# Optimization experiments

Measured on AMD Instinct MI355X. Metric: run time of the kernel, lower is better.

Reference implementation:

```python
import jax, jax.numpy as jnp
import numpy as np

TOP_K = 2


def setup_inputs() -> dict:
    key = jax.random.key(0)
    ks = jax.random.split(key, 5)
    B, S, D, F, E = 2, 2048, 1024, 3584, 8
    scale_in = 1.0 / np.sqrt(D)
    scale_ff = 1.0 / np.sqrt(F)
    return {
        "hidden_states": jax.random.normal(ks[0], (B, S, D), dtype=jnp.float32),
        "gate_w": jax.random.normal(ks[1], (E, D), dtype=jnp.float32) * scale_in,
        "w1": jax.random.normal(ks[2], (E, F, D), dtype=jnp.float32) * scale_in,
        "w3": jax.random.normal(ks[3], (E, F, D), dtype=jnp.float32) * scale_in,
        "w2": jax.random.normal(ks[4], (E, D, F), dtype=jnp.float32) * scale_ff,
    }


def reference(hidden_states, gate_w, w1, w3, w2):
    B, S, D = hidden_states.shape
    E = gate_w.shape[0]
    x = hidden_states.reshape(-1, D)                      # [T, D]
    T = x.shape[0]
    router_logits = x @ gate_w.T                          # [T, E]
    probs = jax.nn.softmax(router_logits.astype(jnp.float32), axis=-1)
    top_w, sel = jax.lax.top_k(probs, TOP_K)              # [T, K]
    top_w = top_w / jnp.sum(top_w, axis=-1, keepdims=True)
    top_w = top_w.astype(x.dtype)
    # per-token per-expert combine weight (scatter top-k weights to dense [T, E])
    w_full = jnp.zeros((T, E), dtype=x.dtype).at[jnp.arange(T)[:, None], sel].add(top_w)
    # Original scales the INPUT by the routing weight before the SwiGLU expert;
    # tokens not routed to expert e have weight 0 -> MLP_e(0) == 0 (no biases),
    # so a dense per-expert pass summed over experts reproduces the gather/scatter exactly.
    out = jnp.zeros_like(x)
    for e in range(E):  # fixed small expert count
        xs = x * w_full[:, e:e + 1]                       # [T, D]
        h = jax.nn.silu(xs @ w1[e].T) * (xs @ w3[e].T)    # [T, F]
        out = out + h @ w2[e].T                           # [T, D]
    return out.reshape(B, S, D), router_logits
```

## Files before the change

### kernel.cpp

```cpp
#include <hip/hip_runtime.h>


#define T_TOK 4096
#define D_DIM 1024
#define F_DIM 3584
#define E_NUM 8
#define N13   (2 * F_DIM)
#define BM 128
#define BN 128
#define BK 32
#define LDK (BK + 8)
#define MAXROWS (2 * T_TOK + E_NUM * (BM - 1) + 8)

typedef __bf16 bf16x8 __attribute__((ext_vector_type(8)));
typedef float  f32x4  __attribute__((ext_vector_type(4)));

__device__ __forceinline__ unsigned f2bf_u(float f) {
    unsigned u = __builtin_bit_cast(unsigned, f);
    return (u + 0x7FFFu + ((u >> 16) & 1u)) >> 16;
}
__device__ __forceinline__ unsigned pack2(float lo, float hi) {
    return f2bf_u(lo) | (f2bf_u(hi) << 16);
}
__device__ __forceinline__ int expert_off(const int* __restrict__ counts, int e) {
    int off = 0;
    for (int i = 0; i < e; i++) off += (counts[i] + BM - 1) & ~(BM - 1);
    return off;
}

__global__ __launch_bounds__(256)
void router(const float* __restrict__ x, const float* __restrict__ gw,
            float* __restrict__ logits, int* __restrict__ counts,
            int* __restrict__ tok, float* __restrict__ wgt)
{
    const int wave = threadIdx.x >> 6;
    const int lane = threadIdx.x & 63;
    const int t = blockIdx.x * 4 + wave;

    const float* xt = x + (size_t)t * D_DIM + lane * 16;
    float4 xv[4];
#pragma unroll
    for (int i = 0; i < 4; i++) xv[i] = ((const float4*)xt)[i];

    float l[E_NUM];
#pragma unroll
    for (int e = 0; e < E_NUM; e++) {
        const float4* gp = (const float4*)(gw + (size_t)e * D_DIM + lane * 16);
        float d = 0.f;
#pragma unroll
        for (int i = 0; i < 4; i++) {
            float4 g = gp[i];
            d += xv[i].x * g.x + xv[i].y * g.y + xv[i].z * g.z + xv[i].w * g.w;
        }
#pragma unroll
        for (int off = 32; off; off >>= 1) d += __shfl_xor(d, off);
        l[e] = d;
    }
#pragma unroll
    for (int e = 0; e < E_NUM; e++)
        if (lane == e) logits[(size_t)t * E_NUM + e] = l[e];

    int e0 = 0; float v0 = l[0];
#pragma unroll
    for (int e = 1; e < E_NUM; e++) if (l[e] > v0) { v0 = l[e]; e0 = e; }
    int e1 = 0; float v1 = -3.4e38f;
#pragma unroll
    for (int e = 0; e < E_NUM; e++) if (e != e0 && l[e] > v1) { v1 = l[e]; e1 = e; }
    const float p1 = __expf(v1 - v0);
    const float w0 = 1.f / (1.f + p1);
    const float w1 = p1 * w0;

    if (lane < 2) {
        const int   ek = lane ? e1 : e0;
        const float wk = lane ? w1 : w0;
        const int pos = atomicAdd(&counts[ek], 1);
        tok[ek * T_TOK + pos] = t;
        wgt[ek * T_TOK + pos] = wk;
    }
}

__global__ __launch_bounds__(256)
void gather(const float* __restrict__ x, const int* __restrict__ counts,
            const int* __restrict__ tok, const float* __restrict__ wgt,
            unsigned short* __restrict__ Xe)
{
    const int e = blockIdx.y;
    const int cnt = counts[e];
    const int cntpad = (cnt + BM - 1) & ~(BM - 1);
    const int r0 = blockIdx.x * BM;
    if (r0 >= cntpad) return;
    const int moff = expert_off(counts, e);

    const int tid = threadIdx.x;
    const int chunk = tid & 63;
    const int rsub = tid >> 6;
#pragma unroll
    for (int i = 0; i < 32; i++) {
        const int r = r0 + rsub + i * 4;
        unsigned short* dst = Xe + (size_t)(moff + r) * D_DIM + chunk * 16;
        uint4 o0 = {0,0,0,0}, o1 = {0,0,0,0};
        if (r < cnt) {
            const int t = tok[e * T_TOK + r];
            const float w = wgt[e * T_TOK + r];
            const float4* src = (const float4*)(x + (size_t)t * D_DIM + chunk * 16);
            float4 a = src[0], b = src[1], c = src[2], d = src[3];
            o0.x = pack2(a.x*w, a.y*w); o0.y = pack2(a.z*w, a.w*w);
            o0.z = pack2(b.x*w, b.y*w); o0.w = pack2(b.z*w, b.w*w);
            o1.x = pack2(c.x*w, c.y*w); o1.y = pack2(c.z*w, c.w*w);
            o1.z = pack2(d.x*w, d.y*w); o1.w = pack2(d.z*w, d.w*w);
        }
        ((uint4*)dst)[0] = o0; ((uint4*)dst)[1] = o1;
    }
}

__global__ __launch_bounds__(256)
void moe_gemm1(const unsigned short* __restrict__ Xe,
               const float* __restrict__ w1, const float* __restrict__ w3,
               const int* __restrict__ counts, unsigned short* __restrict__ H)
{
    const int e = blockIdx.z;
    const int cnt = counts[e];
    const int m0 = blockIdx.y * BM;
    if (m0 >= cnt) return;
    const int moff = expert_off(counts, e);
    const int n0 = blockIdx.x * BN;

    const float* W1 = w1 + (size_t)e * F_DIM * D_DIM;
    const float* W3 = w3 + (size_t)e * F_DIM * D_DIM;

    __shared__ unsigned short As[BM * LDK];
    __shared__ unsigned short Bs[BN * LDK];

    const int tid = threadIdx.x;
    const int lane = tid & 63, wave = tid >> 6;
    const int wm = (wave >> 1) * 64, wn = (wave & 1) * 64;
    const int sr = tid >> 1, sc = (tid & 1) * 16;

    const unsigned short* arow = Xe + (size_t)(moff + m0 + sr) * D_DIM + sc;

    const int ng = n0 + sr;
    const int blk = ng >> 5, rem = ng & 31;
    const float* brow = (rem < 16)
        ? (W1 + (size_t)(blk * 16 + rem) * D_DIM + sc)
        : (W3 + (size_t)(blk * 16 + rem - 16) * D_DIM + sc);

    f32x4 acc[4][4] = {};
    const int ko = (lane >> 4) * 8;
    const int mr = wm + (lane & 15);
    const int nr = wn + (lane & 15);

    for (int k0 = 0; k0 < D_DIM; k0 += BK) {
        uint4 a0 = ((const uint4*)(arow + k0))[0];
        uint4 a1 = ((const uint4*)(arow + k0))[1];
        const float4* bp = (const float4*)(brow + k0);
        float4 b0 = bp[0], b1 = bp[1], b2 = bp[2], b3 = bp[3];
        uint4 pb0, pb1;
        pb0.x = pack2(b0.x, b0.y); pb0.y = pack2(b0.z, b0.w);
        pb0.z = pack2(b1.x, b1.y); pb0.w = pack2(b1.z, b1.w);
        pb1.x = pack2(b2.x, b2.y); pb1.y = pack2(b2.z, b2.w);
        pb1.z = pack2(b3.x, b3.y); pb1.w = pack2(b3.z, b3.w);

        __syncthreads();
        ((uint4*)&As[sr * LDK + sc])[0] = a0;
        ((uint4*)&As[sr * LDK + sc])[1] = a1;
        ((uint4*)&Bs[sr * LDK + sc])[0] = pb0;
        ((uint4*)&Bs[sr * LDK + sc])[1] = pb1;
        __syncthreads();

        bf16x8 af[4], bfm[4];
#pragma unroll
        for (int i = 0; i < 4; i++) {
            af[i]  = *(const bf16x8*)&As[(mr + i * 16) * LDK + ko];
            bfm[i] = *(const bf16x8*)&Bs[(nr + i * 16) * LDK + ko];
        }
#pragma unroll
        for (int mi = 0; mi < 4; mi++)
#pragma unroll
            for (int ni = 0; ni < 4; ni++)
                acc[mi][ni] = __builtin_amdgcn_mfma_f32_16x16x32_bf16(
                    af[mi], bfm[ni], acc[mi][ni], 0, 0, 0);
    }

    const int fb = ((n0 + wn) >> 1) + (lane & 15);
#pragma unroll
    for (int mi = 0; mi < 4; mi++) {
        const int mrow = moff + m0 + wm + mi * 16 + ((lane >> 4) << 2);
#pragma unroll
        for (int p = 0; p < 2; p++) {
            f32x4 g = acc[mi][2 * p];
            f32x4 u = acc[mi][2 * p + 1];
            const int f = fb + p * 16;
#pragma unroll
            for (int r = 0; r < 4; r++) {
                float gv = g[r];
                float hv = (gv / (1.f + __expf(-gv))) * u[r];
                H[(size_t)(mrow + r) * F_DIM + f] = (unsigned short)f2bf_u(hv);
            }
        }
    }
}

__global__ __launch_bounds__(256)
void moe_gemm2(const unsigned short* __restrict__ H, const float* __restrict__ w2,
               const int* __restrict__ counts, const int* __restrict__ tok,
               float* __restrict__ out)
{
    const int e = blockIdx.z;
    const int cnt = counts[e];
    const int m0 = blockIdx.y * BM;
    if (m0 >= cnt) return;
    const int moff = expert_off(counts, e);
    const int n0 = blockIdx.x * BN;

    const float* W2 = w2 + (size_t)e * D_DIM * F_DIM;
    const int* tk = tok + e * T_TOK;

    __shared__ unsigned short As[BM * LDK];
    __shared__ unsigned short Bs[BN * LDK];

    const int tid = threadIdx.x;
    const int lane = tid & 63, wave = tid >> 6;
    const int wm = (wave >> 1) * 64, wn = (wave & 1) * 64;
    const int sr = tid >> 1, sc = (tid & 1) * 16;

    const unsigned short* arow = H + (size_t)(moff + m0 + sr) * F_DIM + sc;
    const float* brow = W2 + (size_t)(n0 + sr) * F_DIM + sc;

    f32x4 acc[4][4] = {};
    const int ko = (lane >> 4) * 8;
    const int mr = wm + (lane & 15);
    const int nr = wn + (lane & 15);

    for (int k0 = 0; k0 < F_DIM; k0 += BK) {
        uint4 a0 = ((const uint4*)(arow + k0))[0];
        uint4 a1 = ((const uint4*)(arow + k0))[1];
        const float4* bp = (const float4*)(brow + k0);
        float4 b0 = bp[0], b1 = bp[1], b2 = bp[2], b3 = bp[3];
        uint4 pb0, pb1;
        pb0.x = pack2(b0.x, b0.y); pb0.y = pack2(b0.z, b0.w);
        pb0.z = pack2(b1.x, b1.y); pb0.w = pack2(b1.z, b1.w);
        pb1.x = pack2(b2.x, b2.y); pb1.y = pack2(b2.z, b2.w);
        pb1.z = pack2(b3.x, b3.y); pb1.w = pack2(b3.z, b3.w);

        __syncthreads();
        ((uint4*)&As[sr * LDK + sc])[0] = a0;
        ((uint4*)&As[sr * LDK + sc])[1] = a1;
        ((uint4*)&Bs[sr * LDK + sc])[0] = pb0;
        ((uint4*)&Bs[sr * LDK + sc])[1] = pb1;
        __syncthreads();

        bf16x8 af[4], bfm[4];
#pragma unroll
        for (int i = 0; i < 4; i++) {
            af[i]  = *(const bf16x8*)&As[(mr + i * 16) * LDK + ko];
            bfm[i] = *(const bf16x8*)&Bs[(nr + i * 16) * LDK + ko];
        }
#pragma unroll
        for (int mi = 0; mi < 4; mi++)
#pragma unroll
            for (int ni = 0; ni < 4; ni++)
                acc[mi][ni] = __builtin_amdgcn_mfma_f32_16x16x32_bf16(
                    af[mi], bfm[ni], acc[mi][ni], 0, 0, 0);
    }

#pragma unroll
    for (int mi = 0; mi < 4; mi++) {
        const int mbase = m0 + wm + mi * 16 + ((lane >> 4) << 2);
#pragma unroll
        for (int r = 0; r < 4; r++) {
            const int m = mbase + r;
            if (m < cnt) {
                const int t = tk[m];
                float* orow = out + (size_t)t * D_DIM + n0 + wn + (lane & 15);
#pragma unroll
                for (int ni = 0; ni < 4; ni++)
                    atomicAdd(orow + ni * 16, acc[mi][ni][r]);
            }
        }
    }
}

extern "C" void kernel_launch(void* const* d_in, const int* in_sizes, int n_in,
                              void* d_out, int out_size, void* d_ws, size_t ws_size,
                              hipStream_t stream)
{
    const float* x  = (const float*)d_in[0];
    const float* gw = (const float*)d_in[1];
    const float* w1 = (const float*)d_in[2];
    const float* w3 = (const float*)d_in[3];
    const float* w2 = (const float*)d_in[4];
    float* out    = (float*)d_out;
    float* logits = out + (size_t)T_TOK * D_DIM;

    char* ws = (char*)d_ws;
    int*   counts = (int*)ws;
    int*   tok    = (int*)(ws + 256);
    float* wgt    = (float*)(ws + 256 + E_NUM * T_TOK * 4);
    unsigned short* Xe = (unsigned short*)(ws + 256 + 2 * E_NUM * T_TOK * 4);
    unsigned short* H  = Xe + (size_t)MAXROWS * D_DIM;

    hipMemsetAsync(out, 0, (size_t)T_TOK * D_DIM * sizeof(float), stream);
    hipMemsetAsync(counts, 0, E_NUM * sizeof(int), stream);

    router<<<T_TOK / 4, 256, 0, stream>>>(x, gw, logits, counts, tok, wgt);
    gather<<<dim3(T_TOK / BM, E_NUM), 256, 0, stream>>>(x, counts, tok, wgt, Xe);
    moe_gemm1<<<dim3(N13 / BN, T_TOK / BM, E_NUM), 256, 0, stream>>>(Xe, w1, w3, counts, H);
    moe_gemm2<<<dim3(D_DIM / BN, T_TOK / BM, E_NUM), 256, 0, stream>>>(H, w2, counts, tok, out);
}
```

Before: 833.8 us.

## Pre-convert weights to bf16, load via global_load_lds, replace atomics with slot buffer

Adds kernels that convert w1/w3 (interleaved) and w2 to bf16 once per call. The GEMMs then stream bf16 tiles straight into LDS with global_load_lds instead of loading fp32 and packing in registers. The down-projection writes each token's two expert contributions to separate slots, tagged by a bit packed into tok, and a combine kernel sums them, removing the atomics and the output memset. The conversion adds a full pass over the fp32 weights plus bf16 writes each call. It needs a large workspace and falls back to the old path when the workspace is too small.

```diff
diff --git a/kernel.cpp b/kernel.cpp
--- a/kernel.cpp
+++ b/kernel.cpp
@@ -10,7 +10,7 @@
 #define BN 128
 #define BK 32
 #define LDK (BK + 8)
-#define MAXROWS (2 * T_TOK + E_NUM * (BM - 1) + 8)
+#define MAXROWS 9216
 
 typedef __bf16 bf16x8 __attribute__((ext_vector_type(8)));
 typedef float  f32x4  __attribute__((ext_vector_type(4)));
@@ -27,6 +27,11 @@
     for (int i = 0; i < e; i++) off += (counts[i] + BM - 1) & ~(BM - 1);
     return off;
 }
+__device__ __forceinline__ void load_lds16(const void* g, void* l) {
+    __builtin_amdgcn_global_load_lds(
+        (const __attribute__((address_space(1))) unsigned*)g,
+        (__attribute__((address_space(3))) unsigned*)l, 16, 0, 0);
+}
 
 __global__ __launch_bounds__(256)
 void router(const float* __restrict__ x, const float* __restrict__ gw,
@@ -74,7 +79,7 @@
         const int   ek = lane ? e1 : e0;
         const float wk = lane ? w1 : w0;
         const int pos = atomicAdd(&counts[ek], 1);
-        tok[ek * T_TOK + pos] = t;
+        tok[ek * T_TOK + pos] = (t << 1) | lane;
         wgt[ek * T_TOK + pos] = wk;
     }
 }
@@ -100,7 +105,7 @@
         unsigned short* dst = Xe + (size_t)(moff + r) * D_DIM + chunk * 16;
         uint4 o0 = {0,0,0,0}, o1 = {0,0,0,0};
         if (r < cnt) {
-            const int t = tok[e * T_TOK + r];
+            const int t = tok[e * T_TOK + r] >> 1;
             const float w = wgt[e * T_TOK + r];
             const float4* src = (const float4*)(x + (size_t)t * D_DIM + chunk * 16);
             float4 a = src[0], b = src[1], c = src[2], d = src[3];
@@ -114,9 +119,41 @@
 }
 
 __global__ __launch_bounds__(256)
-void moe_gemm1(const unsigned short* __restrict__ Xe,
-               const float* __restrict__ w1, const float* __restrict__ w3,
-               const int* __restrict__ counts, unsigned short* __restrict__ H)
+void conv_w13(const float* __restrict__ w1, const float* __restrict__ w3,
+              unsigned short* __restrict__ W13)
+{
+    const size_t idx = (size_t)blockIdx.x * 256 + threadIdx.x;
+    const size_t c = idx * 8;
+    const int col = (int)(c & (D_DIM - 1));
+    const int r   = (int)(c >> 10);
+    const int e   = r / N13;
+    const int ng  = r - e * N13;
+    const int blk = ng >> 5, rem = ng & 31;
+    const float* src = ((rem < 16) ? w1 : w3)
+        + ((size_t)e * F_DIM + blk * 16 + (rem & 15)) * D_DIM + col;
+    float4 a = ((const float4*)src)[0], b = ((const float4*)src)[1];
+    uint4 o;
+    o.x = pack2(a.x, a.y); o.y = pack2(a.z, a.w);
+    o.z = pack2(b.x, b.y); o.w = pack2(b.z, b.w);
+    *(uint4*)(W13 + c) = o;
+}
+
+__global__ __launch_bounds__(256)
+void conv_w2(const float* __restrict__ w2, unsigned short* __restrict__ W2)
+{
+    const size_t idx = (size_t)blockIdx.x * 256 + threadIdx.x;
+    const size_t c = idx * 8;
+    float4 a = ((const float4*)(w2 + c))[0], b = ((const float4*)(w2 + c))[1];
+    uint4 o;
+    o.x = pack2(a.x, a.y); o.y = pack2(a.z, a.w);
+    o.z = pack2(b.x, b.y); o.w = pack2(b.z, b.w);
+    *(uint4*)(W2 + c) = o;
+}
+
+__global__ __launch_bounds__(256)
+void gemm1_bf(const unsigned short* __restrict__ Xe,
+              const unsigned short* __restrict__ W13,
+              const int* __restrict__ counts, unsigned short* __restrict__ H)
 {
     const int e = blockIdx.z;
     const int cnt = counts[e];
@@ -125,6 +162,161 @@
     const int moff = expert_off(counts, e);
     const int n0 = blockIdx.x * BN;
 
+    __shared__ unsigned short As[BM * BK];
+    __shared__ unsigned short Bs[BN * BK];
+
+    const int tid = threadIdx.x, lane = tid & 63, wave = tid >> 6;
+    const int wm = (wave >> 1) * 64, wn = (wave & 1) * 64;
+
+    const int lrow = lane >> 2, lch = (lane & 3) * 8;
+    const unsigned short* gA0 = Xe + (size_t)(moff + m0 + wave * 16 + lrow) * D_DIM + lch;
+    const unsigned short* gA1 = gA0 + (size_t)64 * D_DIM;
+    const unsigned short* gB0 = W13 + ((size_t)e * N13 + n0 + wave * 16 + lrow) * D_DIM + lch;
+    const unsigned short* gB1 = gB0 + (size_t)64 * D_DIM;
+    unsigned short* lA0 = &As[(wave * 16) * BK];
+    unsigned short* lA1 = &As[(64 + wave * 16) * BK];
+    unsigned short* lB0 = &Bs[(wave * 16) * BK];
+    unsigned short* lB1 = &Bs[(64 + wave * 16) * BK];
+
+    f32x4 acc[4][4] = {};
+    const int ko = (lane >> 4) * 8;
+    const int mr = wm + (lane & 15), nr = wn + (lane & 15);
+
+    for (int k0 = 0; k0 < D_DIM; k0 += BK) {
+        load_lds16(gA0, lA0); load_lds16(gA1, lA1);
+        load_lds16(gB0, lB0); load_lds16(gB1, lB1);
+        gA0 += BK; gA1 += BK; gB0 += BK; gB1 += BK;
+        __syncthreads();
+
+        bf16x8 af[4], bfm[4];
+#pragma unroll
+        for (int i = 0; i < 4; i++) {
+            af[i]  = *(const bf16x8*)&As[(mr + i * 16) * BK + ko];
+            bfm[i] = *(const bf16x8*)&Bs[(nr + i * 16) * BK + ko];
+        }
+#pragma unroll
+        for (int mi = 0; mi < 4; mi++)
+#pragma unroll
+            for (int ni = 0; ni < 4; ni++)
+                acc[mi][ni] = __builtin_amdgcn_mfma_f32_16x16x32_bf16(
+                    af[mi], bfm[ni], acc[mi][ni], 0, 0, 0);
+        __syncthreads();
+    }
+
+    const int fb = ((n0 + wn) >> 1) + (lane & 15);
+#pragma unroll
+    for (int mi = 0; mi < 4; mi++) {
+        const int mrow = moff + m0 + wm + mi * 16 + ((lane >> 4) << 2);
+#pragma unroll
+        for (int p = 0; p < 2; p++) {
+            f32x4 g = acc[mi][2 * p];
+            f32x4 u = acc[mi][2 * p + 1];
+            const int f = fb + p * 16;
+#pragma unroll
+            for (int r = 0; r < 4; r++) {
+                float gv = g[r];
+                float hv = (gv / (1.f + __expf(-gv))) * u[r];
+                H[(size_t)(mrow + r) * F_DIM + f] = (unsigned short)f2bf_u(hv);
+            }
+        }
+    }
+}
+
+__global__ __launch_bounds__(256)
+void gemm2_bf(const unsigned short* __restrict__ H,
+              const unsigned short* __restrict__ W2,
+              const int* __restrict__ counts, const int* __restrict__ tok,
+              float* __restrict__ buf)
+{
+    const int e = blockIdx.z;
+    const int cnt = counts[e];
+    const int m0 = blockIdx.y * BM;
+    if (m0 >= cnt) return;
+    const int moff = expert_off(counts, e);
+    const int n0 = blockIdx.x * BN;
+    const int* tk = tok + e * T_TOK;
+
+    __shared__ unsigned short As[BM * BK];
+    __shared__ unsigned short Bs[BN * BK];
+
+    const int tid = threadIdx.x, lane = tid & 63, wave = tid >> 6;
+    const int wm = (wave >> 1) * 64, wn = (wave & 1) * 64;
+
+    const int lrow = lane >> 2, lch = (lane & 3) * 8;
+    const unsigned short* gA0 = H + (size_t)(moff + m0 + wave * 16 + lrow) * F_DIM + lch;
+    const unsigned short* gA1 = gA0 + (size_t)64 * F_DIM;
+    const unsigned short* gB0 = W2 + ((size_t)e * D_DIM + n0 + wave * 16 + lrow) * F_DIM + lch;
+    const unsigned short* gB1 = gB0 + (size_t)64 * F_DIM;
+    unsigned short* lA0 = &As[(wave * 16) * BK];
+    unsigned short* lA1 = &As[(64 + wave * 16) * BK];
+    unsigned short* lB0 = &Bs[(wave * 16) * BK];
+    unsigned short* lB1 = &Bs[(64 + wave * 16) * BK];
+
+    f32x4 acc[4][4] = {};
+    const int ko = (lane >> 4) * 8;
+    const int mr = wm + (lane & 15), nr = wn + (lane & 15);
+
+    for (int k0 = 0; k0 < F_DIM; k0 += BK) {
+        load_lds16(gA0, lA0); load_lds16(gA1, lA1);
+        load_lds16(gB0, lB0); load_lds16(gB1, lB1);
+        gA0 += BK; gA1 += BK; gB0 += BK; gB1 += BK;
+        __syncthreads();
+
+        bf16x8 af[4], bfm[4];
+#pragma unroll
+        for (int i = 0; i < 4; i++) {
+            af[i]  = *(const bf16x8*)&As[(mr + i * 16) * BK + ko];
+            bfm[i] = *(const bf16x8*)&Bs[(nr + i * 16) * BK + ko];
+        }
+#pragma unroll
+        for (int mi = 0; mi < 4; mi++)
+#pragma unroll
+            for (int ni = 0; ni < 4; ni++)
+                acc[mi][ni] = __builtin_amdgcn_mfma_f32_16x16x32_bf16(
+                    af[mi], bfm[ni], acc[mi][ni], 0, 0, 0);
+        __syncthreads();
+    }
+
+#pragma unroll
+    for (int mi = 0; mi < 4; mi++) {
+        const int mbase = m0 + wm + mi * 16 + ((lane >> 4) << 2);
+#pragma unroll
+        for (int r = 0; r < 4; r++) {
+            const int m = mbase + r;
+            if (m < cnt) {
+                const int v = tk[m];
+                float* orow = buf + ((size_t)(v & 1) * T_TOK + (v >> 1)) * D_DIM
+                            + n0 + wn + (lane & 15);
+#pragma unroll
+                for (int ni = 0; ni < 4; ni++)
+                    orow[ni * 16] = acc[mi][ni][r];
+            }
+        }
+    }
+}
+
+__global__ __launch_bounds__(256)
+void combine(const float* __restrict__ buf, float* __restrict__ out)
+{
+    const size_t i = (size_t)blockIdx.x * 256 + threadIdx.x;
+    float4 a = ((const float4*)buf)[i];
+    float4 b = ((const float4*)(buf + (size_t)T_TOK * D_DIM))[i];
+    float4 o = {a.x + b.x, a.y + b.y, a.z + b.z, a.w + b.w};
+    ((float4*)out)[i] = o;
+}
+
+__global__ __launch_bounds__(256)
+void legacy_gemm1(const unsigned short* __restrict__ Xe,
+                  const float* __restrict__ w1, const float* __restrict__ w3,
+                  const int* __restrict__ counts, unsigned short* __restrict__ H)
+{
+    const int e = blockIdx.z;
+    const int cnt = counts[e];
+    const int m0 = blockIdx.y * BM;
+    if (m0 >= cnt) return;
+    const int moff = expert_off(counts, e);
+    const int n0 = blockIdx.x * BN;
+
     const float* W1 = w1 + (size_t)e * F_DIM * D_DIM;
     const float* W3 = w3 + (size_t)e * F_DIM * D_DIM;
 
@@ -137,7 +329,6 @@
     const int sr = tid >> 1, sc = (tid & 1) * 16;
 
     const unsigned short* arow = Xe + (size_t)(moff + m0 + sr) * D_DIM + sc;
-
     const int ng = n0 + sr;
     const int blk = ng >> 5, rem = ng & 31;
     const float* brow = (rem < 16)
@@ -201,9 +392,9 @@
 }
 
 __global__ __launch_bounds__(256)
-void moe_gemm2(const unsigned short* __restrict__ H, const float* __restrict__ w2,
-               const int* __restrict__ counts, const int* __restrict__ tok,
-               float* __restrict__ out)
+void legacy_gemm2(const unsigned short* __restrict__ H, const float* __restrict__ w2,
+                  const int* __restrict__ counts, const int* __restrict__ tok,
+                  float* __restrict__ out)
 {
     const int e = blockIdx.z;
     const int cnt = counts[e];
@@ -270,7 +461,7 @@
         for (int r = 0; r < 4; r++) {
             const int m = mbase + r;
             if (m < cnt) {
-                const int t = tk[m];
+                const int t = tk[m] >> 1;
                 float* orow = out + (size_t)t * D_DIM + n0 + wn + (lane & 15);
 #pragma unroll
                 for (int ni = 0; ni < 4; ni++)
@@ -295,15 +486,27 @@
     char* ws = (char*)d_ws;
     int*   counts = (int*)ws;
     int*   tok    = (int*)(ws + 256);
-    float* wgt    = (float*)(ws + 256 + E_NUM * T_TOK * 4);
-    unsigned short* Xe = (unsigned short*)(ws + 256 + 2 * E_NUM * T_TOK * 4);
-    unsigned short* H  = Xe + (size_t)MAXROWS * D_DIM;
-
-    hipMemsetAsync(out, 0, (size_t)T_TOK * D_DIM * sizeof(float), stream);
+    float* wgt    = (float*)(ws + 131328);
+    unsigned short* Xe = (unsigned short*)(ws + 262400);
+    unsigned short* H  = (unsigned short*)(ws + 19136768);
+    float*          buf = (float*)(ws + 85197056);
+    unsigned short* W13 = (unsigned short*)(ws + 118751488);
+    unsigned short* W2b = (unsigned short*)(ws + 236192000);
+    const size_t NEED_FULL = 294912256;
+
     hipMemsetAsync(counts, 0, E_NUM * sizeof(int), stream);
-
     router<<<T_TOK / 4, 256, 0, stream>>>(x, gw, logits, counts, tok, wgt);
     gather<<<dim3(T_TOK / BM, E_NUM), 256, 0, stream>>>(x, counts, tok, wgt, Xe);
-    moe_gemm1<<<dim3(N13 / BN, T_TOK / BM, E_NUM), 256, 0, stream>>>(Xe, w1, w3, counts, H);
-    moe_gemm2<<<dim3(D_DIM / BN, T_TOK / BM, E_NUM), 256, 0, stream>>>(H, w2, counts, tok, out);
-}
+
+    if (ws_size >= NEED_FULL) {
+        conv_w13<<<(E_NUM * (size_t)N13 * D_DIM / 8) / 256, 256, 0, stream>>>(w1, w3, W13);
+        conv_w2<<<(E_NUM * (size_t)D_DIM * F_DIM / 8) / 256, 256, 0, stream>>>(w2, W2b);
+        gemm1_bf<<<dim3(N13 / BN, T_TOK / BM, E_NUM), 256, 0, stream>>>(Xe, W13, counts, H);
+        gemm2_bf<<<dim3(D_DIM / BN, T_TOK / BM, E_NUM), 256, 0, stream>>>(H, W2b, counts, tok, buf);
+        combine<<<(T_TOK * D_DIM / 4) / 256, 256, 0, stream>>>(buf, out);
+    } else {
+        hipMemsetAsync(out, 0, (size_t)T_TOK * D_DIM * sizeof(float), stream);
+        legacy_gemm1<<<dim3(N13 / BN, T_TOK / BM, E_NUM), 256, 0, stream>>>(Xe, w1, w3, counts, H);
+        legacy_gemm2<<<dim3(D_DIM / BN, T_TOK / BM, E_NUM), 256, 0, stream>>>(H, w2, counts, tok, out);
+    }
+}
```

New measurement: 770.2 us. 1.08x faster.
